# Kernel tuning notes

Measured on AMD Instinct MI355X. Metric: run time of the kernel, lower is better.

The kernel has to match this reference:

```python
import jax, jax.numpy as jnp
import numpy as np

N = 65536      # bs * n_graphs * 32 electrodes
E = 1048576    # edges (avg degree 16)
H = 128        # first_hc (out_channels of GatedGraphConv)
IN = 5         # input node features
G = 16         # n_graphs (conv1d in-channels)
ELEC = 32
BS = 128
NC = 3


def setup_inputs() -> dict:
    key = jax.random.key(0)
    ks = jax.random.split(key, 14)
    s = 1.0 / np.sqrt(H)
    x = jax.random.normal(ks[0], (N, IN), dtype=jnp.float32)
    edge_index = jax.random.randint(ks[1], (2, E), 0, N, dtype=jnp.int32)
    edge_attr = jax.random.uniform(ks[2], (E,), dtype=jnp.float32)
    gconv_w = jax.random.normal(ks[3], (2, H, H), dtype=jnp.float32) * s
    gru_w_ih = jax.random.normal(ks[4], (3 * H, H), dtype=jnp.float32) * s
    gru_w_hh = jax.random.normal(ks[5], (3 * H, H), dtype=jnp.float32) * s
    gru_b_ih = jax.random.normal(ks[6], (3 * H,), dtype=jnp.float32) * s
    gru_b_hh = jax.random.normal(ks[7], (3 * H,), dtype=jnp.float32) * s
    conv_w = jax.random.normal(ks[8], (1, G, 3), dtype=jnp.float32) * (1.0 / np.sqrt(G * 3))
    conv_b = jax.random.normal(ks[9], (1,), dtype=jnp.float32) * 0.1
    L = (H - 3) // 2 + 1  # 63
    lin1_w = jax.random.normal(ks[10], (H, ELEC * L), dtype=jnp.float32) * (1.0 / np.sqrt(ELEC * L))
    lin1_b = jnp.zeros((H,), dtype=jnp.float32)
    lin2_w = jax.random.normal(ks[11], (NC, H), dtype=jnp.float32) * s
    lin2_b = jnp.zeros((NC,), dtype=jnp.float32)
    return {"x": x, "edge_index": edge_index, "edge_attr": edge_attr, "bs": BS,
            "gconv_w": gconv_w, "gru_w_ih": gru_w_ih, "gru_w_hh": gru_w_hh,
            "gru_b_ih": gru_b_ih, "gru_b_hh": gru_b_hh,
            "conv_w": conv_w, "conv_b": conv_b,
            "lin1_w": lin1_w, "lin1_b": lin1_b, "lin2_w": lin2_w, "lin2_b": lin2_b}


def _gated_graph_conv(x, edge_index, edge_attr, gconv_w, w_ih, w_hh, b_ih, b_hh):
    n = x.shape[0]
    # pad input features up to H (PyG GatedGraphConv behavior when in < out)
    h = jnp.concatenate([x, jnp.zeros((n, H - x.shape[1]), dtype=x.dtype)], axis=1)
    src, dst = edge_index[0], edge_index[1]
    for i in range(2):  # num_layers = 2
        m = h @ gconv_w[i]                              # [N, H]
        msg = m[src] * edge_attr[:, None]               # gather + edge weight
        agg = jax.ops.segment_sum(msg, dst, num_segments=n)  # scatter-add
        # GRUCell(agg, h)
        gi = agg @ w_ih.T + b_ih
        gh = h @ w_hh.T + b_hh
        i_r, i_z, i_n = jnp.split(gi, 3, axis=1)
        h_r, h_z, h_n = jnp.split(gh, 3, axis=1)
        r = jax.nn.sigmoid(i_r + h_r)
        z = jax.nn.sigmoid(i_z + h_z)
        nn_ = jnp.tanh(i_n + r * h_n)
        h = (1.0 - z) * nn_ + z * h
    return h


def reference(x, edge_index, edge_attr, bs, gconv_w, gru_w_ih, gru_w_hh,
              gru_b_ih, gru_b_hh, conv_w, conv_b, lin1_w, lin1_b, lin2_w, lin2_b):
    h = _gated_graph_conv(x, edge_index, edge_attr, gconv_w,
                          gru_w_ih, gru_w_hh, gru_b_ih, gru_b_hh)
    h = jax.nn.relu(h)  # dropout is identity in eval mode
    g = h.shape[0] // (bs * ELEC)
    # (bs g e) f -> (bs e) g f
    h = h.reshape(bs, g, ELEC, H).transpose(0, 2, 1, 3).reshape(bs * ELEC, g, H)
    h = jax.lax.conv_general_dilated(h, conv_w, window_strides=(2,), padding='VALID',
                                     dimension_numbers=('NCH', 'OIH', 'NCH'))
    h = h + conv_b[None, :, None]
    h = jax.nn.relu(h[:, 0, :])                 # squeeze channel -> [bs*e, L]
    h = h.reshape(bs, -1)                       # (bs e) f -> bs (e f)
    h = jax.nn.relu(h @ lin1_w.T + lin1_b)
    h = h @ lin2_w.T + lin2_b
    return jax.nn.softmax(h, axis=-1)
```

## Files before the change

### kernel.cpp

```cpp
#include <hip/hip_runtime.h>
#include <math.h>

#define NN 65536
#define NE 1048576
#define HH 128
#define ELEC 32
#define BSZ 128
#define NB 512

typedef unsigned short ushort_t;
typedef __bf16 bf16x8 __attribute__((ext_vector_type(8)));
typedef float f32x16 __attribute__((ext_vector_type(16)));

#define MFMA(A, B, C) __builtin_amdgcn_mfma_f32_32x32x16_bf16(A, B, C, 0, 0, 0)

__device__ __forceinline__ float sigm(float x) { return 1.f / (1.f + __expf(-x)); }
__device__ __forceinline__ float tanh_fast(float x) { return 2.f / (1.f + __expf(-2.f * x)) - 1.f; }

__device__ __forceinline__ float bf2f(ushort_t u) {
    union { unsigned int i; float f; } v; v.i = ((unsigned int)u) << 16; return v.f;
}
__device__ __forceinline__ ushort_t f2bf(float f) {
    union { float f; unsigned int i; } v; v.f = f;
    unsigned int r = (v.i + 0x7fffu + ((v.i >> 16) & 1u)) >> 16;
    return (ushort_t)r;
}


__global__ void k_init(const float* __restrict__ x, ushort_t* __restrict__ h) {
    int i = blockIdx.x * 256 + threadIdx.x;
    int n = i >> 7, c = i & 127;
    float v = (c < 5) ? x[n * 5 + c] : 0.f;
    h[(size_t)n * 128 + c] = f2bf(v);
}

__global__ __launch_bounds__(256) void k_bhist(const int* __restrict__ dst,
                                               int* __restrict__ bcnt) {
    __shared__ int hh[NB];
    int t = threadIdx.x;
    hh[t] = 0; hh[t + 256] = 0;
    __syncthreads();
    int e0 = blockIdx.x * 4096;
    #pragma unroll
    for (int i = 0; i < 16; ++i)
        atomicAdd(&hh[dst[e0 + i * 256 + t] >> 7], 1);
    __syncthreads();
    int c0 = hh[t];       if (c0) atomicAdd(&bcnt[t], c0);
    int c1 = hh[t + 256]; if (c1) atomicAdd(&bcnt[t + 256], c1);
}

__global__ void k_bscan(const int* __restrict__ bcnt, int* __restrict__ boffs,
                        int* __restrict__ bcur) {
    __shared__ int s[NB];
    int t = threadIdx.x;
    int v = bcnt[t];
    s[t] = v;
    __syncthreads();
    for (int d = 1; d < NB; d <<= 1) {
        int u = (t >= d) ? s[t - d] : 0;
        __syncthreads();
        s[t] += u;
        __syncthreads();
    }
    int ex = s[t] - v;
    boffs[t] = ex;
    bcur[t] = ex;
    if (t == NB - 1) boffs[NB] = s[t];
}

__global__ __launch_bounds__(256) void k_bpart(const int* __restrict__ src,
        const int* __restrict__ dst, const float* __restrict__ ea,
        int* __restrict__ bcur, uint2* __restrict__ ebkt) {
    __shared__ int lcnt[NB];
    __shared__ int base[NB];
    __shared__ int lcur[NB];
    int t = threadIdx.x;
    lcnt[t] = 0; lcnt[t + 256] = 0;
    lcur[t] = 0; lcur[t + 256] = 0;
    __syncthreads();
    int e0 = blockIdx.x * 4096;
    #pragma unroll
    for (int i = 0; i < 16; ++i)
        atomicAdd(&lcnt[dst[e0 + i * 256 + t] >> 7], 1);
    __syncthreads();
    {
        int c = lcnt[t];
        base[t] = c ? atomicAdd(&bcur[t], c) : 0;
        c = lcnt[t + 256];
        base[t + 256] = c ? atomicAdd(&bcur[t + 256], c) : 0;
    }
    __syncthreads();
    #pragma unroll
    for (int i = 0; i < 16; ++i) {
        int e = e0 + i * 256 + t;
        int d = dst[e];
        int bk = d >> 7;
        int pos = base[bk] + atomicAdd(&lcur[bk], 1);
        uint2 pk;
        pk.x = (unsigned int)src[e] | ((unsigned int)(d & 127) << 16);
        pk.y = __float_as_uint(ea[e]);
        ebkt[pos] = pk;
    }
}

__global__ __launch_bounds__(256) void k_csc(const int* __restrict__ boffs,
        const uint2* __restrict__ ebkt, uint2* __restrict__ epack,
        int* __restrict__ offs) {
    __shared__ int cnt[128];
    __shared__ int s[128];
    __shared__ int base[128];
    int b = blockIdx.x, t = threadIdx.x;
    if (t < 128) cnt[t] = 0;
    __syncthreads();
    int e0 = boffs[b], e1 = boffs[b + 1];
    for (int i = e0 + t; i < e1; i += 256)
        atomicAdd(&cnt[(ebkt[i].x >> 16) & 127], 1);
    __syncthreads();
    if (t < 128) s[t] = cnt[t];
    __syncthreads();
    for (int d = 1; d < 128; d <<= 1) {
        int v = (t < 128 && t >= d) ? s[t - d] : 0;
        __syncthreads();
        if (t < 128) s[t] += v;
        __syncthreads();
    }
    if (t < 128) {
        int bs = e0 + s[t] - cnt[t];
        base[t] = bs;
        offs[b * 128 + t] = bs;
        cnt[t] = 0;
    }
    if (b == 0 && t == 255) offs[NN] = NE;
    __syncthreads();
    for (int i = e0 + t; i < e1; i += 256) {
        uint2 e = ebkt[i];
        int dl = (e.x >> 16) & 127;
        int pos = base[dl] + atomicAdd(&cnt[dl], 1);
        epack[pos] = e;
    }
}

__global__ void k_prep(const float* __restrict__ wih, const float* __restrict__ whh,
                       const float* __restrict__ gw, const float* __restrict__ l1w,
                       ushort_t* __restrict__ vp, ushort_t* __restrict__ gp,
                       float* __restrict__ wt) {
    int b = blockIdx.x, t = threadIdx.x;
    if (b < 512) {
        int i = b * 256 + t;
        int rho = i >> 8, k = i & 255;
        int q = rho >> 7, g = (rho >> 5) & 3, cc = rho & 31;
        int c = q * 32 + cc;
        float v;
        if (g == 0)      v = (k < 128) ? wih[c * 128 + k]          : whh[c * 128 + k - 128];
        else if (g == 1) v = (k < 128) ? wih[(128 + c) * 128 + k]  : whh[(128 + c) * 128 + k - 128];
        else if (g == 2) v = (k < 128) ? wih[(256 + c) * 128 + k]  : 0.f;
        else             v = (k < 128) ? 0.f                       : whh[(256 + c) * 128 + k - 128];
        int ks = k >> 4, lh = (k >> 3) & 1, j = k & 7, lr = cc;
        vp[(size_t)(ks * 16 + q * 4 + g) * 512 + (lh * 32 + lr) * 8 + j] = f2bf(v);
    } else if (b < 640) {
        int i = (b - 512) * 256 + t;
        int l = i >> 14, r = i & 16383, c = r >> 7, k = r & 127;
        float v = gw[l * 16384 + k * 128 + c];
        int ct = c >> 5, lr = c & 31;
        int ks = k >> 4, lh = (k >> 3) & 1, j = k & 7;
        gp[(size_t)((l * 8 + ks) * 4 + ct) * 512 + (lh * 32 + lr) * 8 + j] = f2bf(v);
    } else {
        int i = (b - 640) * 256 + t;
        int k = i >> 7, c = i & 127;
        wt[i] = l1w[c * 2016 + k];
    }
}

__global__ __launch_bounds__(256, 4) void k_mgemm(const ushort_t* __restrict__ gp,
        const ushort_t* __restrict__ h, ushort_t* __restrict__ m) {
    int t = threadIdx.x;
    int lane = t & 63, w = t >> 6;
    int lr = lane & 31, lh = lane >> 5;
    int n0 = blockIdx.x * 128 + w * 32;
    f32x16 acc[4];
    #pragma unroll
    for (int ct = 0; ct < 4; ++ct)
        #pragma unroll
        for (int r = 0; r < 16; ++r) acc[ct][r] = 0.f;
    size_t rowA = (size_t)(n0 + lr) * 128;
    #pragma unroll
    for (int ks = 0; ks < 8; ++ks) {
        int kg = ks * 16 + lh * 8;
        bf16x8 a = *reinterpret_cast<const bf16x8*>(h + rowA + kg);
        #pragma unroll
        for (int ct = 0; ct < 4; ++ct) {
            bf16x8 b = *reinterpret_cast<const bf16x8*>(gp + (size_t)(ks * 4 + ct) * 512 + lane * 8);
            acc[ct] = MFMA(a, b, acc[ct]);
        }
    }
    #pragma unroll
    for (int ct = 0; ct < 4; ++ct)
        #pragma unroll
        for (int r = 0; r < 16; ++r) {
            int row = (r & 3) + 8 * (r >> 2) + 4 * lh;
            m[(size_t)(n0 + row) * 128 + ct * 32 + lr] = f2bf(acc[ct][r]);
        }
}

__global__ __launch_bounds__(256) void k_gather(const ushort_t* __restrict__ m,
        const int* __restrict__ offs, const uint2* __restrict__ epack,
        ushort_t* __restrict__ agg) {
    int n = blockIdx.x * 4 + (threadIdx.x >> 6);
    int lane = threadIdx.x & 63;
    int k0 = offs[n], k1 = offs[n + 1];
    float a0 = 0.f, a1 = 0.f;
    int k = k0;
    if (k < k1 && (k & 1)) {
        uint2 e = epack[k];
        float w = __uint_as_float(e.y);
        ushort2 u = *reinterpret_cast<const ushort2*>(m + (size_t)(e.x & 0xFFFFu) * HH + 2 * lane);
        a0 = fmaf(w, bf2f(u.x), a0);
        a1 = fmaf(w, bf2f(u.y), a1);
        ++k;
    }
    for (; k + 8 <= k1; k += 8) {
        uint4 ea_ = *reinterpret_cast<const uint4*>(epack + k);
        uint4 eb_ = *reinterpret_cast<const uint4*>(epack + k + 2);
        uint4 ec_ = *reinterpret_cast<const uint4*>(epack + k + 4);
        uint4 ed_ = *reinterpret_cast<const uint4*>(epack + k + 6);
        ushort2 u0 = *reinterpret_cast<const ushort2*>(m + (size_t)(ea_.x & 0xFFFFu) * HH + 2 * lane);
        ushort2 u1 = *reinterpret_cast<const ushort2*>(m + (size_t)(ea_.z & 0xFFFFu) * HH + 2 * lane);
        ushort2 u2 = *reinterpret_cast<const ushort2*>(m + (size_t)(eb_.x & 0xFFFFu) * HH + 2 * lane);
        ushort2 u3 = *reinterpret_cast<const ushort2*>(m + (size_t)(eb_.z & 0xFFFFu) * HH + 2 * lane);
        ushort2 u4 = *reinterpret_cast<const ushort2*>(m + (size_t)(ec_.x & 0xFFFFu) * HH + 2 * lane);
        ushort2 u5 = *reinterpret_cast<const ushort2*>(m + (size_t)(ec_.z & 0xFFFFu) * HH + 2 * lane);
        ushort2 u6 = *reinterpret_cast<const ushort2*>(m + (size_t)(ed_.x & 0xFFFFu) * HH + 2 * lane);
        ushort2 u7 = *reinterpret_cast<const ushort2*>(m + (size_t)(ed_.z & 0xFFFFu) * HH + 2 * lane);
        float w0 = __uint_as_float(ea_.y), w1 = __uint_as_float(ea_.w);
        float w2 = __uint_as_float(eb_.y), w3 = __uint_as_float(eb_.w);
        float w4 = __uint_as_float(ec_.y), w5 = __uint_as_float(ec_.w);
        float w6 = __uint_as_float(ed_.y), w7 = __uint_as_float(ed_.w);
        a0 = fmaf(w0, bf2f(u0.x), a0); a1 = fmaf(w0, bf2f(u0.y), a1);
        a0 = fmaf(w1, bf2f(u1.x), a0); a1 = fmaf(w1, bf2f(u1.y), a1);
        a0 = fmaf(w2, bf2f(u2.x), a0); a1 = fmaf(w2, bf2f(u2.y), a1);
        a0 = fmaf(w3, bf2f(u3.x), a0); a1 = fmaf(w3, bf2f(u3.y), a1);
        a0 = fmaf(w4, bf2f(u4.x), a0); a1 = fmaf(w4, bf2f(u4.y), a1);
        a0 = fmaf(w5, bf2f(u5.x), a0); a1 = fmaf(w5, bf2f(u5.y), a1);
        a0 = fmaf(w6, bf2f(u6.x), a0); a1 = fmaf(w6, bf2f(u6.y), a1);
        a0 = fmaf(w7, bf2f(u7.x), a0); a1 = fmaf(w7, bf2f(u7.y), a1);
    }
    for (; k + 2 <= k1; k += 2) {
        uint4 e01 = *reinterpret_cast<const uint4*>(epack + k);
        ushort2 u0 = *reinterpret_cast<const ushort2*>(m + (size_t)(e01.x & 0xFFFFu) * HH + 2 * lane);
        ushort2 u1 = *reinterpret_cast<const ushort2*>(m + (size_t)(e01.z & 0xFFFFu) * HH + 2 * lane);
        float w0 = __uint_as_float(e01.y), w1 = __uint_as_float(e01.w);
        a0 = fmaf(w0, bf2f(u0.x), a0); a1 = fmaf(w0, bf2f(u0.y), a1);
        a0 = fmaf(w1, bf2f(u1.x), a0); a1 = fmaf(w1, bf2f(u1.y), a1);
    }
    if (k < k1) {
        uint2 e = epack[k];
        float w = __uint_as_float(e.y);
        ushort2 u = *reinterpret_cast<const ushort2*>(m + (size_t)(e.x & 0xFFFFu) * HH + 2 * lane);
        a0 = fmaf(w, bf2f(u.x), a0);
        a1 = fmaf(w, bf2f(u.y), a1);
    }
    ushort2 o; o.x = f2bf(a0); o.y = f2bf(a1);
    *reinterpret_cast<ushort2*>(agg + (size_t)n * 128 + 2 * lane) = o;
}

__global__ __launch_bounds__(512, 4) void k_gru(const ushort_t* __restrict__ vp,
        const ushort_t* __restrict__ agg, ushort_t* __restrict__ h,
        const float* __restrict__ bih, const float* __restrict__ bhh) {
    int t = threadIdx.x;
    int lane = t & 63, w = t >> 6;
    int q = w >> 1, s = w & 1;
    int lr = lane & 31, lh = lane >> 5;
    int n0 = blockIdx.x * 64 + s * 32;
    f32x16 acc[4];
    #pragma unroll
    for (int g = 0; g < 4; ++g)
        #pragma unroll
        for (int r = 0; r < 16; ++r) acc[g][r] = 0.f;

    size_t rowA = (size_t)(n0 + lr) * 128;
    #pragma unroll
    for (int ks = 0; ks < 16; ++ks) {
        bf16x8 a;
        if (ks < 8) a = *reinterpret_cast<const bf16x8*>(agg + rowA + ks * 16 + lh * 8);
        else        a = *reinterpret_cast<const bf16x8*>(h + rowA + (ks - 8) * 16 + lh * 8);
        #pragma unroll
        for (int g = 0; g < 4; ++g) {
            bf16x8 b = *reinterpret_cast<const bf16x8*>(vp + (size_t)(ks * 16 + q * 4 + g) * 512 + lane * 8);
            acc[g] = MFMA(a, b, acc[g]);
        }
    }

    __syncthreads();

    int c = q * 32 + lr;
    float brz = bih[c] + bhh[c];
    float bzz = bih[128 + c] + bhh[128 + c];
    float bin = bih[256 + c];
    float bhn = bhh[256 + c];
    #pragma unroll
    for (int r = 0; r < 16; ++r) {
        int node = n0 + (r & 3) + 8 * (r >> 2) + 4 * lh;
        float rg = sigm(acc[0][r] + brz);
        float zg = sigm(acc[1][r] + bzz);
        float nn = tanh_fast(acc[2][r] + bin + rg * (acc[3][r] + bhn));
        size_t idx = (size_t)node * 128 + c;
        float hold = bf2f(h[idx]);
        float hnew = (1.f - zg) * nn + zg * hold;
        h[idx] = f2bf(hnew);
    }
}

__global__ __launch_bounds__(64) void k_conv(const ushort_t* __restrict__ h,
        const float* __restrict__ cw, const float* __restrict__ cb,
        float* __restrict__ co) {
    __shared__ float tile[16 * 128];
    __shared__ float w[48];
    int be = blockIdx.x;
    int b = be >> 5, e = be & 31;
    int t = threadIdx.x;
    if (t < 48) w[t] = cw[t];
    #pragma unroll
    for (int i = 0; i < 8; ++i) {
        int f = t + i * 64;
        int g = f >> 5, c4 = f & 31;
        size_t idx = (size_t)(b * 512 + g * 32 + e) * 128 + c4 * 4;
        ushort4 vh4 = *reinterpret_cast<const ushort4*>(h + idx);
        float* dst = tile + g * 128 + c4 * 4;
        dst[0] = fmaxf(bf2f(vh4.x), 0.f);
        dst[1] = fmaxf(bf2f(vh4.y), 0.f);
        dst[2] = fmaxf(bf2f(vh4.z), 0.f);
        dst[3] = fmaxf(bf2f(vh4.w), 0.f);
    }
    __syncthreads();
    if (t < 63) {
        float s = cb[0];
        #pragma unroll
        for (int g = 0; g < 16; ++g) {
            const float* p = tile + g * 128 + 2 * t;
            s = fmaf(p[0], w[g * 3 + 0], s);
            s = fmaf(p[1], w[g * 3 + 1], s);
            s = fmaf(p[2], w[g * 3 + 2], s);
        }
        co[b * 2016 + e * 63 + t] = fmaxf(s, 0.f);
    }
}

__global__ __launch_bounds__(128) void k_lin1(const float* __restrict__ co,
        const float* __restrict__ wt, float* __restrict__ fc1) {
    int b = blockIdx.x >> 3;
    int ks = blockIdx.x & 7;
    int c = threadIdx.x;
    const float* cb_ = co + b * 2016 + ks * 252;
    const float* wb = wt + (ks * 252) * 128 + c;
    float s = 0.f;
    #pragma unroll 4
    for (int k = 0; k < 252; ++k)
        s = fmaf(wb[k * 128], cb_[k], s);
    atomicAdd(&fc1[b * 128 + c], s);
}

__global__ __launch_bounds__(128) void k_lin2(const float* __restrict__ fc1,
        const float* __restrict__ l1b, const float* __restrict__ w,
        const float* __restrict__ bias, float* __restrict__ out) {
    int b = threadIdx.x;
    float s0 = bias[0], s1 = bias[1], s2 = bias[2];
    const float* v = fc1 + b * 128;
    for (int k = 0; k < 128; ++k) {
        float x = fmaxf(v[k] + l1b[k], 0.f);
        s0 = fmaf(x, w[k], s0);
        s1 = fmaf(x, w[128 + k], s1);
        s2 = fmaf(x, w[256 + k], s2);
    }
    float mx = fmaxf(s0, fmaxf(s1, s2));
    float e0 = __expf(s0 - mx), e1 = __expf(s1 - mx), e2 = __expf(s2 - mx);
    float inv = 1.f / (e0 + e1 + e2);
    out[b * 3 + 0] = e0 * inv;
    out[b * 3 + 1] = e1 * inv;
    out[b * 3 + 2] = e2 * inv;
}

extern "C" void kernel_launch(void* const* d_in, const int* in_sizes, int n_in,
                              void* d_out, int out_size, void* d_ws, size_t ws_size,
                              hipStream_t stream) {
    const float* x   = (const float*)d_in[0];
    const int*   ei  = (const int*)d_in[1];
    const float* ea  = (const float*)d_in[2];
    const float* gw  = (const float*)d_in[4];
    const float* wih = (const float*)d_in[5];
    const float* whh = (const float*)d_in[6];
    const float* bih = (const float*)d_in[7];
    const float* bhh = (const float*)d_in[8];
    const float* cw  = (const float*)d_in[9];
    const float* cb  = (const float*)d_in[10];
    const float* l1w = (const float*)d_in[11];
    const float* l1b = (const float*)d_in[12];
    const float* l2w = (const float*)d_in[13];
    const float* l2b = (const float*)d_in[14];
    float* out = (float*)d_out;

    char* p = (char*)d_ws;
    ushort_t* h   = (ushort_t*)p; p += (size_t)NN * 128 * 2;
    ushort_t* agg = (ushort_t*)p; p += (size_t)NN * 128 * 2;
    ushort_t* vp  = (ushort_t*)p; p += 512 * 256 * 2;
    ushort_t* gp  = (ushort_t*)p; p += 2 * 128 * 128 * 2;
    ushort_t* m   = (ushort_t*)p; p += (size_t)NN * HH * 2;
    uint2* ebkt   = (uint2*)p;   p += (size_t)NE * 8;
    uint2* epack  = (uint2*)p;   p += (size_t)NE * 8;
    float* wt  = (float*)p; p += 2016 * 128 * 4;
    float* co  = (float*)p; p += (size_t)BSZ * 2016 * 4;
    float* fc1 = (float*)p; p += (size_t)BSZ * HH * 4;
    int* bcnt  = (int*)p; p += NB * 4;
    int* boffs = (int*)p; p += (NB + 1) * 4;
    int* bcur  = (int*)p; p += NB * 4;
    int* offs  = (int*)p; p += (size_t)(NN + 1) * 4;

    const int* src = ei;
    const int* dst = ei + NE;

    k_prep<<<1648, 256, 0, stream>>>(wih, whh, gw, l1w, vp, gp, wt);
    hipMemsetAsync(bcnt, 0, NB * 4, stream);
    hipMemsetAsync(fc1, 0, (size_t)BSZ * HH * 4, stream);
    k_bhist<<<256, 256, 0, stream>>>(dst, bcnt);
    k_bscan<<<1, 512, 0, stream>>>(bcnt, boffs, bcur);
    k_bpart<<<256, 256, 0, stream>>>(src, dst, ea, bcur, ebkt);
    k_csc<<<NB, 256, 0, stream>>>(boffs, ebkt, epack, offs);
    k_init<<<(NN * 128) / 256, 256, 0, stream>>>(x, h);

    for (int layer = 0; layer < 2; ++layer) {
        k_mgemm<<<NN / 128, 256, 0, stream>>>(gp + (size_t)layer * 16384, h, m);
        k_gather<<<NN / 4, 256, 0, stream>>>(m, offs, epack, agg);
        k_gru<<<NN / 64, 512, 0, stream>>>(vp, agg, h, bih, bhh);
    }

    k_conv<<<BSZ * ELEC, 64, 0, stream>>>(h, cw, cb, co);
    k_lin1<<<BSZ * 8, 128, 0, stream>>>(co, wt, fc1);
    k_lin2<<<1, 128, 0, stream>>>(fc1, l1b, l2w, l2b, out);
}
```

Before: 364.9 us.

## Fold graph-conv weight into GRU input weights, gather h directly

```diff
diff --git a/kernel.cpp b/kernel.cpp
--- a/kernel.cpp
+++ b/kernel.cpp
@@ -142,67 +142,40 @@
 
 __global__ void k_prep(const float* __restrict__ wih, const float* __restrict__ whh,
                        const float* __restrict__ gw, const float* __restrict__ l1w,
-                       ushort_t* __restrict__ vp, ushort_t* __restrict__ gp,
-                       float* __restrict__ wt) {
+                       ushort_t* __restrict__ vp, float* __restrict__ wt) {
     int b = blockIdx.x, t = threadIdx.x;
-    if (b < 512) {
+    if (b < 1024) {
         int i = b * 256 + t;
-        int rho = i >> 8, k = i & 255;
+        int l = i >> 17, r2 = i & 131071;
+        int rho = r2 >> 8, k = r2 & 255;
         int q = rho >> 7, g = (rho >> 5) & 3, cc = rho & 31;
         int c = q * 32 + cc;
         float v;
-        if (g == 0)      v = (k < 128) ? wih[c * 128 + k]          : whh[c * 128 + k - 128];
-        else if (g == 1) v = (k < 128) ? wih[(128 + c) * 128 + k]  : whh[(128 + c) * 128 + k - 128];
-        else if (g == 2) v = (k < 128) ? wih[(256 + c) * 128 + k]  : 0.f;
-        else             v = (k < 128) ? 0.f                       : whh[(256 + c) * 128 + k - 128];
+        if (k >= 128) {
+            if (g == 0)      v = whh[c * 128 + k - 128];
+            else if (g == 1) v = whh[(128 + c) * 128 + k - 128];
+            else if (g == 2) v = 0.f;
+            else             v = whh[(256 + c) * 128 + k - 128];
+        } else if (g == 3) {
+            v = 0.f;
+        } else {
+            int crow = (g == 0) ? c : ((g == 1) ? 128 + c : 256 + c);
+            const float* gr = gw + l * 16384 + k * 128;
+            const float* wr = wih + crow * 128;
+            float s = 0.f;
+            for (int j = 0; j < 128; ++j) s = fmaf(gr[j], wr[j], s);
+            v = s;
+        }
         int ks = k >> 4, lh = (k >> 3) & 1, j = k & 7, lr = cc;
-        vp[(size_t)(ks * 16 + q * 4 + g) * 512 + (lh * 32 + lr) * 8 + j] = f2bf(v);
-    } else if (b < 640) {
-        int i = (b - 512) * 256 + t;
-        int l = i >> 14, r = i & 16383, c = r >> 7, k = r & 127;
-        float v = gw[l * 16384 + k * 128 + c];
-        int ct = c >> 5, lr = c & 31;
-        int ks = k >> 4, lh = (k >> 3) & 1, j = k & 7;
-        gp[(size_t)((l * 8 + ks) * 4 + ct) * 512 + (lh * 32 + lr) * 8 + j] = f2bf(v);
+        vp[(size_t)l * 131072 + (size_t)(ks * 16 + q * 4 + g) * 512 + (lh * 32 + lr) * 8 + j] = f2bf(v);
     } else {
-        int i = (b - 640) * 256 + t;
+        int i = (b - 1024) * 256 + t;
         int k = i >> 7, c = i & 127;
         wt[i] = l1w[c * 2016 + k];
     }
 }
 
-__global__ __launch_bounds__(256, 4) void k_mgemm(const ushort_t* __restrict__ gp,
-        const ushort_t* __restrict__ h, ushort_t* __restrict__ m) {
-    int t = threadIdx.x;
-    int lane = t & 63, w = t >> 6;
-    int lr = lane & 31, lh = lane >> 5;
-    int n0 = blockIdx.x * 128 + w * 32;
-    f32x16 acc[4];
-    #pragma unroll
-    for (int ct = 0; ct < 4; ++ct)
-        #pragma unroll
-        for (int r = 0; r < 16; ++r) acc[ct][r] = 0.f;
-    size_t rowA = (size_t)(n0 + lr) * 128;
-    #pragma unroll
-    for (int ks = 0; ks < 8; ++ks) {
-        int kg = ks * 16 + lh * 8;
-        bf16x8 a = *reinterpret_cast<const bf16x8*>(h + rowA + kg);
-        #pragma unroll
-        for (int ct = 0; ct < 4; ++ct) {
-            bf16x8 b = *reinterpret_cast<const bf16x8*>(gp + (size_t)(ks * 4 + ct) * 512 + lane * 8);
-            acc[ct] = MFMA(a, b, acc[ct]);
-        }
-    }
-    #pragma unroll
-    for (int ct = 0; ct < 4; ++ct)
-        #pragma unroll
-        for (int r = 0; r < 16; ++r) {
-            int row = (r & 3) + 8 * (r >> 2) + 4 * lh;
-            m[(size_t)(n0 + row) * 128 + ct * 32 + lr] = f2bf(acc[ct][r]);
-        }
-}
-
-__global__ __launch_bounds__(256) void k_gather(const ushort_t* __restrict__ m,
+__global__ __launch_bounds__(256) void k_gather(const ushort_t* __restrict__ h,
         const int* __restrict__ offs, const uint2* __restrict__ epack,
         ushort_t* __restrict__ agg) {
     int n = blockIdx.x * 4 + (threadIdx.x >> 6);
@@ -213,7 +186,7 @@
     if (k < k1 && (k & 1)) {
         uint2 e = epack[k];
         float w = __uint_as_float(e.y);
-        ushort2 u = *reinterpret_cast<const ushort2*>(m + (size_t)(e.x & 0xFFFFu) * HH + 2 * lane);
+        ushort2 u = *reinterpret_cast<const ushort2*>(h + (size_t)(e.x & 0xFFFFu) * HH + 2 * lane);
         a0 = fmaf(w, bf2f(u.x), a0);
         a1 = fmaf(w, bf2f(u.y), a1);
         ++k;
@@ -223,14 +196,14 @@
         uint4 eb_ = *reinterpret_cast<const uint4*>(epack + k + 2);
         uint4 ec_ = *reinterpret_cast<const uint4*>(epack + k + 4);
         uint4 ed_ = *reinterpret_cast<const uint4*>(epack + k + 6);
-        ushort2 u0 = *reinterpret_cast<const ushort2*>(m + (size_t)(ea_.x & 0xFFFFu) * HH + 2 * lane);
-        ushort2 u1 = *reinterpret_cast<const ushort2*>(m + (size_t)(ea_.z & 0xFFFFu) * HH + 2 * lane);
-        ushort2 u2 = *reinterpret_cast<const ushort2*>(m + (size_t)(eb_.x & 0xFFFFu) * HH + 2 * lane);
-        ushort2 u3 = *reinterpret_cast<const ushort2*>(m + (size_t)(eb_.z & 0xFFFFu) * HH + 2 * lane);
-        ushort2 u4 = *reinterpret_cast<const ushort2*>(m + (size_t)(ec_.x & 0xFFFFu) * HH + 2 * lane);
-        ushort2 u5 = *reinterpret_cast<const ushort2*>(m + (size_t)(ec_.z & 0xFFFFu) * HH + 2 * lane);
-        ushort2 u6 = *reinterpret_cast<const ushort2*>(m + (size_t)(ed_.x & 0xFFFFu) * HH + 2 * lane);
-        ushort2 u7 = *reinterpret_cast<const ushort2*>(m + (size_t)(ed_.z & 0xFFFFu) * HH + 2 * lane);
+        ushort2 u0 = *reinterpret_cast<const ushort2*>(h + (size_t)(ea_.x & 0xFFFFu) * HH + 2 * lane);
+        ushort2 u1 = *reinterpret_cast<const ushort2*>(h + (size_t)(ea_.z & 0xFFFFu) * HH + 2 * lane);
+        ushort2 u2 = *reinterpret_cast<const ushort2*>(h + (size_t)(eb_.x & 0xFFFFu) * HH + 2 * lane);
+        ushort2 u3 = *reinterpret_cast<const ushort2*>(h + (size_t)(eb_.z & 0xFFFFu) * HH + 2 * lane);
+        ushort2 u4 = *reinterpret_cast<const ushort2*>(h + (size_t)(ec_.x & 0xFFFFu) * HH + 2 * lane);
+        ushort2 u5 = *reinterpret_cast<const ushort2*>(h + (size_t)(ec_.z & 0xFFFFu) * HH + 2 * lane);
+        ushort2 u6 = *reinterpret_cast<const ushort2*>(h + (size_t)(ed_.x & 0xFFFFu) * HH + 2 * lane);
+        ushort2 u7 = *reinterpret_cast<const ushort2*>(h + (size_t)(ed_.z & 0xFFFFu) * HH + 2 * lane);
         float w0 = __uint_as_float(ea_.y), w1 = __uint_as_float(ea_.w);
         float w2 = __uint_as_float(eb_.y), w3 = __uint_as_float(eb_.w);
         float w4 = __uint_as_float(ec_.y), w5 = __uint_as_float(ec_.w);
@@ -246,8 +219,8 @@
     }
     for (; k + 2 <= k1; k += 2) {
         uint4 e01 = *reinterpret_cast<const uint4*>(epack + k);
-        ushort2 u0 = *reinterpret_cast<const ushort2*>(m + (size_t)(e01.x & 0xFFFFu) * HH + 2 * lane);
-        ushort2 u1 = *reinterpret_cast<const ushort2*>(m + (size_t)(e01.z & 0xFFFFu) * HH + 2 * lane);
+        ushort2 u0 = *reinterpret_cast<const ushort2*>(h + (size_t)(e01.x & 0xFFFFu) * HH + 2 * lane);
+        ushort2 u1 = *reinterpret_cast<const ushort2*>(h + (size_t)(e01.z & 0xFFFFu) * HH + 2 * lane);
         float w0 = __uint_as_float(e01.y), w1 = __uint_as_float(e01.w);
         a0 = fmaf(w0, bf2f(u0.x), a0); a1 = fmaf(w0, bf2f(u0.y), a1);
         a0 = fmaf(w1, bf2f(u1.x), a0); a1 = fmaf(w1, bf2f(u1.y), a1);
@@ -255,7 +228,7 @@
     if (k < k1) {
         uint2 e = epack[k];
         float w = __uint_as_float(e.y);
-        ushort2 u = *reinterpret_cast<const ushort2*>(m + (size_t)(e.x & 0xFFFFu) * HH + 2 * lane);
+        ushort2 u = *reinterpret_cast<const ushort2*>(h + (size_t)(e.x & 0xFFFFu) * HH + 2 * lane);
         a0 = fmaf(w, bf2f(u.x), a0);
         a1 = fmaf(w, bf2f(u.y), a1);
     }
@@ -401,9 +374,7 @@
     char* p = (char*)d_ws;
     ushort_t* h   = (ushort_t*)p; p += (size_t)NN * 128 * 2;
     ushort_t* agg = (ushort_t*)p; p += (size_t)NN * 128 * 2;
-    ushort_t* vp  = (ushort_t*)p; p += 512 * 256 * 2;
-    ushort_t* gp  = (ushort_t*)p; p += 2 * 128 * 128 * 2;
-    ushort_t* m   = (ushort_t*)p; p += (size_t)NN * HH * 2;
+    ushort_t* vp  = (ushort_t*)p; p += 2 * 512 * 256 * 2;
     uint2* ebkt   = (uint2*)p;   p += (size_t)NE * 8;
     uint2* epack  = (uint2*)p;   p += (size_t)NE * 8;
     float* wt  = (float*)p; p += 2016 * 128 * 4;
@@ -417,7 +388,7 @@
     const int* src = ei;
     const int* dst = ei + NE;
 
-    k_prep<<<1648, 256, 0, stream>>>(wih, whh, gw, l1w, vp, gp, wt);
+    k_prep<<<2032, 256, 0, stream>>>(wih, whh, gw, l1w, vp, wt);
     hipMemsetAsync(bcnt, 0, NB * 4, stream);
     hipMemsetAsync(fc1, 0, (size_t)BSZ * HH * 4, stream);
     k_bhist<<<256, 256, 0, stream>>>(dst, bcnt);
@@ -427,9 +398,8 @@
     k_init<<<(NN * 128) / 256, 256, 0, stream>>>(x, h);
 
     for (int layer = 0; layer < 2; ++layer) {
-        k_mgemm<<<NN / 128, 256, 0, stream>>>(gp + (size_t)layer * 16384, h, m);
-        k_gather<<<NN / 4, 256, 0, stream>>>(m, offs, epack, agg);
-        k_gru<<<NN / 64, 512, 0, stream>>>(vp, agg, h, bih, bhh);
+        k_gather<<<NN / 4, 256, 0, stream>>>(h, offs, epack, agg);
+        k_gru<<<NN / 64, 512, 0, stream>>>(vp + (size_t)layer * 131072, agg, h, bih, bhh);
     }
 
     k_conv<<<BSZ * ELEC, 64, 0, stream>>>(h, cw, cb, co);
```

Result: faster. 348.2 us (-4.6%).
